# Kernel optimization log

Hardware: AMD Instinct MI355X
Metric: run time of the kernel (lower is better)

Reference implementation:

```python
import jax, jax.numpy as jnp
from jax import lax
import numpy as np

B, N, S, K, C = 8, 16384, 1024, 32, 256


def setup_inputs() -> dict:
    key = jax.random.key(0)
    ks = jax.random.split(key, 8)
    def lin(k, o, i):
        return (jax.random.normal(k, (o, i), jnp.float32) / np.sqrt(i)).astype(jnp.float32)
    return {
        "x": jax.random.normal(ks[0], (B, N, 3), jnp.float32),
        "Wqkv": lin(ks[1], 3 * C, 3), "bqkv": jnp.zeros((3 * C,), jnp.float32),
        "g1": lin(ks[2], C, C), "bg1": jnp.zeros((C,), jnp.float32),
        "g2": lin(ks[3], C, C), "bg2": jnp.zeros((C,), jnp.float32),
        "Wo": lin(ks[4], C, C), "bo": jnp.zeros((C,), jnp.float32),
        "p1": lin(ks[5], 128, 3), "bp1": jnp.zeros((128,), jnp.float32),
        "p2": lin(ks[6], C, 128), "bp2": jnp.zeros((C,), jnp.float32),
    }


def _fps(xyz, num_patches):
    # furthest point sampling, deterministic start at index 0 (matches pointnet2 CUDA op)
    b, n, _ = xyz.shape
    def body(carry, _):
        dmin, far = carry
        c = jnp.take_along_axis(xyz, far[:, None, None], axis=1)[:, 0]  # [B,3]
        d = jnp.sum((xyz - c[:, None, :]) ** 2, axis=-1)                # [B,N]
        dmin = jnp.minimum(dmin, d)
        return (dmin, jnp.argmax(dmin, axis=-1)), far
    init = (jnp.full((b, n), 1e10, xyz.dtype), jnp.zeros((b,), jnp.int32))
    _, idx = lax.scan(body, init, None, length=num_patches)
    return jnp.transpose(idx)  # [B,S]


def _gelu(x):
    return jax.nn.gelu(x, approximate=False)  # torch nn.GELU default = exact erf


def reference(x, Wqkv, bqkv, g1, bg1, g2, bg2, Wo, bo, p1, bp1, p2, bp2):
    scale = C ** (-0.5)
    fps_idx = _fps(x, S)                                        # [B,S]
    centroid = jnp.take_along_axis(x, fps_idx[..., None], axis=1)  # [B,S,3]
    # square_distance(centroid, x): [B,S,N]
    d = (jnp.sum(centroid ** 2, -1)[..., None]
         + jnp.sum(x ** 2, -1)[:, None, :]
         - 2.0 * jnp.einsum('bsc,bnc->bsn', centroid, x))
    _, knn = lax.top_k(-d, K)                                   # [B,S,K] smallest-k (== argsort[:, :, :k])
    grouped = jax.vmap(lambda pts, i: pts[i])(x, knn)           # [B,S,K,3]
    # 1x1 Conv2d over channel dim == linear on last axis
    qkv = grouped @ Wqkv.T + bqkv                               # [B,S,K,3C]
    q, k_, v = jnp.split(qkv, 3, axis=-1)
    q = q.max(axis=2); k_ = k_.max(axis=2); v = v.max(axis=2)   # [B,S,C]
    h = _gelu((q - k_) @ g1.T + bg1) @ g2.T + bg2               # fc_gamma MLP
    attn = jax.nn.softmax(h * scale, axis=-1)                   # softmax over channels
    pos = _gelu(centroid @ p1.T + bp1) @ p2.T + bp2             # [B,S,C]
    return (attn * v) @ Wo.T + bo + pos                         # [B,S,C]
```

## Files before the change

### kernel.cpp

```cpp
#include <hip/hip_runtime.h>
#include <hip/hip_bf16.h>
#include <cstdint>

#define B_ 8
#define N_ 16384
#define S_ 1024
#define K_ 32
#define C_ 256
#define RR 8

__device__ __forceinline__ float gelu_f(float x){
  return 0.5f * x * (1.0f + erff(x * 0.70710678118654752f));
}

__device__ __forceinline__ float dist2_f(float px, float py, float pz,
                                         float cx, float cy, float cz){
  float dx = px - cx, dy = py - cy, dz = pz - cz;
  return dx*dx + dy*dy + dz*dz;
}

__global__ void prep_kernel(const float* __restrict__ x,
                            const float* __restrict__ g1,
                            const float* __restrict__ g2,
                            const float* __restrict__ Wo,
                            const float* __restrict__ p2,
                            float* __restrict__ xT,
                            float* __restrict__ g1T,
                            float* __restrict__ g2T,
                            float* __restrict__ WoT,
                            float* __restrict__ p2T){
  int u = blockIdx.x * 256 + threadIdx.x;
  if (u < B_*N_){
    int b = u >> 14, n = u & (N_-1);
    const float* p = x + (size_t)u * 3;
    xT[((size_t)b*3+0)*N_ + n] = p[0];
    xT[((size_t)b*3+1)*N_ + n] = p[1];
    xT[((size_t)b*3+2)*N_ + n] = p[2];
  } else if (u < B_*N_ + 65536){
    int v = u - B_*N_; int i = v >> 8, j = v & 255;
    g1T[v] = g1[j*256 + i];
  } else if (u < B_*N_ + 2*65536){
    int v = u - B_*N_ - 65536; int i = v >> 8, j = v & 255;
    g2T[v] = g2[j*256 + i];
  } else if (u < B_*N_ + 3*65536){
    int v = u - B_*N_ - 2*65536; int i = v >> 8, j = v & 255;
    WoT[v] = Wo[j*256 + i];
  } else if (u < B_*N_ + 3*65536 + 32768){
    int v = u - B_*N_ - 3*65536; int i = v >> 8, j = v & 255;
    p2T[v] = p2[j*128 + i];
  }
}

__global__ __launch_bounds__(1024, 4) void fps_kernel(const float* __restrict__ xT,
                                                      float* __restrict__ cent){
  int b = blockIdx.x;
  int tid = threadIdx.x;
  const float* X = xT + (size_t)b*3*N_;
  const float* Y = X + N_;
  const float* Z = Y + N_;
  float px[16], py[16], pz[16], dm[16];
  #pragma unroll
  for (int i=0;i<16;i++){
    int g = i*1024 + tid;
    px[i]=X[g]; py[i]=Y[g]; pz[i]=Z[g]; dm[i]=1e10f;
  }
  __shared__ unsigned mslot[2];
  __shared__ int islot[2];
  if (tid==0){ mslot[0]=0u; mslot[1]=0u; islot[0]=0x7FFFFFFF; islot[1]=0x7FFFFFFF; }
  __syncthreads();
  int far = 0;
  for (int s=0; s<S_; s++){
    int cur = s & 1;
    float cx = X[far], cy = Y[far], cz = Z[far];
    if (tid==0){
      float* o = cent + ((size_t)b*S_ + s)*3;
      o[0]=cx; o[1]=cy; o[2]=cz;
    }
    float m = 0.0f;
    #pragma unroll
    for (int i=0;i<16;i++){
      float d = dist2_f(px[i],py[i],pz[i],cx,cy,cz);
      dm[i] = fminf(dm[i], d);
      m = fmaxf(m, dm[i]);
    }
    for (int off=32; off; off>>=1) m = fmaxf(m, __shfl_xor(m, off));
    if ((tid & 63) == 0) atomicMax(&mslot[cur], __float_as_uint(m));
    __syncthreads();
    float gm = __uint_as_float(mslot[cur]);
    if (m == gm){
      int cand = 0x7FFFFFFF;
      #pragma unroll
      for (int i=15;i>=0;i--) if (dm[i]==gm) cand = i*1024 + tid;
      if (cand != 0x7FFFFFFF) atomicMin(&islot[cur], cand);
    }
    if (tid==0){ mslot[cur^1]=0u; islot[cur^1]=0x7FFFFFFF; }
    __syncthreads();
    far = islot[cur];
  }
}

__global__ __launch_bounds__(256) void knn_qkv_kernel(const float* __restrict__ xT,
                                                      const float* __restrict__ cent,
                                                      const float* __restrict__ Wqkv,
                                                      const float* __restrict__ bqkv,
                                                      float* __restrict__ qkv){
  __shared__ unsigned hist[RR][256];
  __shared__ unsigned candB[RR][256];
  __shared__ int      candI[RR][256];
  __shared__ int      selI[RR][32];
  __shared__ float    pts[RR][32][3];
  __shared__ int      cnt[RR];
  __shared__ int      Bstar[RR];
  int tid = threadIdx.x;
  int row0 = blockIdx.x * RR;
  int b = row0 >> 10;
  const float* X = xT + (size_t)b*3*N_;
  const float* Y = X + N_;
  const float* Z = Y + N_;
  float cx[RR], cy[RR], cz[RR];
  #pragma unroll
  for (int r=0;r<RR;r++){
    const float* c = cent + ((size_t)row0 + r)*3;
    cx[r]=c[0]; cy[r]=c[1]; cz[r]=c[2];
  }
  for (int i=tid; i<RR*256; i+=256) ((unsigned*)hist)[i] = 0u;
  if (tid < RR) cnt[tid]=0;
  __syncthreads();
  for (int i=0;i<64;i++){
    int g = i*256 + tid;
    float px=X[g], py=Y[g], pz=Z[g];
    #pragma unroll
    for (int r=0;r<RR;r++){
      float d = dist2_f(px,py,pz,cx[r],cy[r],cz[r]);
      int key = (int)(__float_as_uint(d) >> 20) - 840;
      key = min(max(key,0),255);
      atomicAdd(&hist[r][key], 1u);
    }
  }
  __syncthreads();
  int w = tid >> 6, lane = tid & 63;
  for (int half=0; half<2; half++){
    int r = half*4 + w;
    uint4 h4 = ((uint4*)&hist[r][0])[lane];
    unsigned cum = h4.x + h4.y + h4.z + h4.w;
    for (int off=1; off<64; off<<=1){
      unsigned t = __shfl_up(cum, off);
      if (lane >= off) cum += t;
    }
    unsigned long long mask = __ballot(cum >= 32u);
    int lb = __ffsll((unsigned long long)mask) - 1;
    unsigned cumPrev = __shfl(cum, lb>0 ? lb-1 : 0);
    if (lane == lb){
      unsigned c0 = (lb==0) ? 0u : cumPrev;
      unsigned hh[4] = {h4.x,h4.y,h4.z,h4.w};
      int bs = lb*4 + 3;
      for (int k=0;k<4;k++){
        if (c0 + hh[k] >= 32u){ bs = lb*4 + k; break; }
        c0 += hh[k];
      }
      Bstar[r] = bs;
    }
  }
  __syncthreads();
  int bsr[RR];
  #pragma unroll
  for (int r=0;r<RR;r++) bsr[r] = min(Bstar[r]+1, 255);
  for (int i=0;i<64;i++){
    int g = i*256 + tid;
    float px=X[g], py=Y[g], pz=Z[g];
    #pragma unroll
    for (int r=0;r<RR;r++){
      float d = dist2_f(px,py,pz,cx[r],cy[r],cz[r]);
      unsigned bits = __float_as_uint(d);
      int key = min(max((int)(bits>>20) - 840, 0), 255);
      if (key <= bsr[r]){
        int pos = atomicAdd(&cnt[r], 1);
        if (pos < 256){ candB[r][pos] = bits; candI[r][pos] = g; }
      }
    }
  }
  __syncthreads();
  for (int half=0; half<2; half++){
    int r = half*4 + w;
    int L = min(cnt[r], 256);
    for (int j=lane; j<L; j+=64){
      unsigned mb = candB[r][j]; int mi = candI[r][j];
      int rank = 0;
      for (int t=0;t<L;t++){
        unsigned tb = candB[r][t]; int ti = candI[r][t];
        rank += (tb < mb || (tb == mb && ti < mi)) ? 1 : 0;
      }
      if (rank < 32) selI[r][rank] = mi;
    }
  }
  __syncthreads();
  { int r = tid >> 5, p = tid & 31;
    int g = selI[r][p];
    pts[r][p][0]=X[g]; pts[r][p][1]=Y[g]; pts[r][p][2]=Z[g]; }
  __syncthreads();
  float w0[3], w1[3], w2[3], bb[3];
  #pragma unroll
  for (int c3=0;c3<3;c3++){
    int c = tid + c3*256;
    w0[c3]=Wqkv[c*3+0]; w1[c3]=Wqkv[c*3+1]; w2[c3]=Wqkv[c*3+2]; bb[c3]=bqkv[c];
  }
  for (int r=0;r<RR;r++){
    float m0=-1e30f, m1=-1e30f, m2=-1e30f;
    #pragma unroll
    for (int p=0;p<32;p++){
      float px=pts[r][p][0], py=pts[r][p][1], pz=pts[r][p][2];
      m0 = fmaxf(m0, w0[0]*px + w1[0]*py + w2[0]*pz);
      m1 = fmaxf(m1, w0[1]*px + w1[1]*py + w2[1]*pz);
      m2 = fmaxf(m2, w0[2]*px + w1[2]*py + w2[2]*pz);
    }
    float* o = qkv + ((size_t)row0 + r)*768;
    o[tid      ] = m0 + bb[0];
    o[tid + 256] = m1 + bb[1];
    o[tid + 512] = m2 + bb[2];
  }
}

template<int KD>
__device__ __forceinline__ void gemm_tile(const float* A_, const float* __restrict__ Wt,
                                          int rb, int lane, float acc[4][4]){
  const float4* W4 = (const float4*)Wt;
  for (int i0=0; i0<(KD>>2); i0++){
    float4 wv0 = W4[(i0*4+0)*64 + lane];
    float4 wv1 = W4[(i0*4+1)*64 + lane];
    float4 wv2 = W4[(i0*4+2)*64 + lane];
    float4 wv3 = W4[(i0*4+3)*64 + lane];
    #pragma unroll
    for (int r=0;r<4;r++){
      float4 a = ((const float4*)(A_ + (size_t)(rb+r)*KD))[i0];
      acc[r][0] = fmaf(a.x,wv0.x,fmaf(a.y,wv1.x,fmaf(a.z,wv2.x,fmaf(a.w,wv3.x,acc[r][0]))));
      acc[r][1] = fmaf(a.x,wv0.y,fmaf(a.y,wv1.y,fmaf(a.z,wv2.y,fmaf(a.w,wv3.y,acc[r][1]))));
      acc[r][2] = fmaf(a.x,wv0.z,fmaf(a.y,wv1.z,fmaf(a.z,wv2.z,fmaf(a.w,wv3.z,acc[r][2]))));
      acc[r][3] = fmaf(a.x,wv0.w,fmaf(a.y,wv1.w,fmaf(a.z,wv2.w,fmaf(a.w,wv3.w,acc[r][3]))));
    }
  }
}

__global__ __launch_bounds__(512, 2) void stage2_kernel(const float* __restrict__ qkv,
                                                        const float* __restrict__ cent,
                                                        const float* __restrict__ g1T,
                                                        const float* __restrict__ bg1,
                                                        const float* __restrict__ g2T,
                                                        const float* __restrict__ bg2,
                                                        const float* __restrict__ WoT,
                                                        const float* __restrict__ bo,
                                                        const float* __restrict__ p1,
                                                        const float* __restrict__ bp1,
                                                        const float* __restrict__ p2T,
                                                        const float* __restrict__ bp2,
                                                        float* __restrict__ out){
  __shared__ float A[32][256];
  __shared__ float T[32][128];
  __shared__ float CC[32][3];
  int tid = threadIdx.x;
  int w = tid >> 6, lane = tid & 63;
  int rb = w * 4;
  int row0 = blockIdx.x * 32;
  const float4* qkv4 = (const float4*)qkv;
  #pragma unroll
  for (int t=0;t<4;t++){
    int fi = t*512 + tid;
    int r = fi >> 6, c4 = fi & 63;
    float4 q = qkv4[(size_t)(row0+r)*192 + c4];
    float4 k = qkv4[(size_t)(row0+r)*192 + 64 + c4];
    ((float4*)&A[r][0])[c4] = make_float4(q.x-k.x, q.y-k.y, q.z-k.z, q.w-k.w);
  }
  if (tid < 96) ((float*)CC)[tid] = cent[(size_t)row0*3 + tid];
  __syncthreads();
  #pragma unroll
  for (int t=0;t<8;t++){
    int e = t*512 + tid;
    int r = e >> 7, c = e & 127;
    float tv = CC[r][0]*p1[c*3+0] + CC[r][1]*p1[c*3+1] + CC[r][2]*p1[c*3+2] + bp1[c];
    T[r][c] = gelu_f(tv);
  }
  __syncthreads();
  float acc[4][4];
  #pragma unroll
  for (int r=0;r<4;r++){ acc[r][0]=0.f; acc[r][1]=0.f; acc[r][2]=0.f; acc[r][3]=0.f; }
  gemm_tile<256>(&A[0][0], g1T, rb, lane, acc);
  {
    float4 bg = ((const float4*)bg1)[lane];
    #pragma unroll
    for (int r=0;r<4;r++){
      float4 g;
      g.x = gelu_f(acc[r][0] + bg.x);
      g.y = gelu_f(acc[r][1] + bg.y);
      g.z = gelu_f(acc[r][2] + bg.z);
      g.w = gelu_f(acc[r][3] + bg.w);
      ((float4*)&A[rb+r][0])[lane] = g;
    }
  }
  #pragma unroll
  for (int r=0;r<4;r++){ acc[r][0]=0.f; acc[r][1]=0.f; acc[r][2]=0.f; acc[r][3]=0.f; }
  gemm_tile<256>(&A[0][0], g2T, rb, lane, acc);
  {
    float4 bg = ((const float4*)bg2)[lane];
    const float scale = 0.0625f;
    #pragma unroll
    for (int r=0;r<4;r++){
      float h0 = acc[r][0]+bg.x, h1 = acc[r][1]+bg.y, h2 = acc[r][2]+bg.z, h3 = acc[r][3]+bg.w;
      float mx = fmaxf(fmaxf(h0,h1), fmaxf(h2,h3));
      for (int off=1; off<64; off<<=1) mx = fmaxf(mx, __shfl_xor(mx, off));
      float e0 = __expf((h0-mx)*scale), e1 = __expf((h1-mx)*scale);
      float e2 = __expf((h2-mx)*scale), e3 = __expf((h3-mx)*scale);
      float sm = e0+e1+e2+e3;
      for (int off=1; off<64; off<<=1) sm += __shfl_xor(sm, off);
      float inv = 1.0f / sm;
      float4 v4 = qkv4[(size_t)(row0+rb+r)*192 + 128 + lane];
      ((float4*)&A[rb+r][0])[lane] =
          make_float4(e0*inv*v4.x, e1*inv*v4.y, e2*inv*v4.z, e3*inv*v4.w);
    }
  }
  #pragma unroll
  for (int r=0;r<4;r++){ acc[r][0]=0.f; acc[r][1]=0.f; acc[r][2]=0.f; acc[r][3]=0.f; }
  gemm_tile<256>(&A[0][0], WoT, rb, lane, acc);
  gemm_tile<128>(&T[0][0], p2T, rb, lane, acc);
  {
    float4 bov = ((const float4*)bo)[lane];
    float4 bpv = ((const float4*)bp2)[lane];
    #pragma unroll
    for (int r=0;r<4;r++){
      float4 o;
      o.x = acc[r][0] + bov.x + bpv.x;
      o.y = acc[r][1] + bov.y + bpv.y;
      o.z = acc[r][2] + bov.z + bpv.z;
      o.w = acc[r][3] + bov.w + bpv.w;
      ((float4*)out)[(size_t)(row0+rb+r)*64 + lane] = o;
    }
  }
}

extern "C" void kernel_launch(void* const* d_in, const int* in_sizes, int n_in,
                              void* d_out, int out_size, void* d_ws, size_t ws_size,
                              hipStream_t stream) {
  const float* x    = (const float*)d_in[0];
  const float* Wqkv = (const float*)d_in[1];
  const float* bqkv = (const float*)d_in[2];
  const float* g1   = (const float*)d_in[3];
  const float* bg1  = (const float*)d_in[4];
  const float* g2   = (const float*)d_in[5];
  const float* bg2  = (const float*)d_in[6];
  const float* Wo   = (const float*)d_in[7];
  const float* bo   = (const float*)d_in[8];
  const float* p1   = (const float*)d_in[9];
  const float* bp1  = (const float*)d_in[10];
  const float* p2   = (const float*)d_in[11];
  const float* bp2  = (const float*)d_in[12];
  float* out = (float*)d_out;
  float* ws = (float*)d_ws;

  float* xT   = ws;
  float* cent = xT + 393216;
  float* qkv  = cent + 24576;
  float* g1T  = qkv + 6291456;
  float* g2T  = g1T + 65536;
  float* WoT  = g2T + 65536;
  float* p2T  = WoT + 65536;

  hipLaunchKernelGGL(prep_kernel, dim3(1408), dim3(256), 0, stream,
                     x, g1, g2, Wo, p2, xT, g1T, g2T, WoT, p2T);
  hipLaunchKernelGGL(fps_kernel, dim3(B_), dim3(1024), 0, stream, xT, cent);
  hipLaunchKernelGGL(knn_qkv_kernel, dim3(B_*S_/RR), dim3(256), 0, stream,
                     xT, cent, Wqkv, bqkv, qkv);
  hipLaunchKernelGGL(stage2_kernel, dim3(B_*S_/32), dim3(512), 0, stream,
                     qkv, cent, g1T, bg1, g2T, bg2, WoT, bo, p1, bp1, p2T, bp2, out);
}
```

Measured before the change: 1.900 ms.

## Restructure FPS kernel with 512 threads, per-wave max slots, and packed float4 points

The FPS kernel now runs 512 threads per batch, each holding 32 points, and reads points from a new packed float4 array written by the prep kernel. The global max is found by writing per-wave maxima to shared memory and reducing them, which replaces the shared atomicMax slot. The next centroid comes from one float4 load instead of three strided loads. Centroids are buffered in shared memory and written out at the end. The intent is to cut per-iteration synchronisation and atomic costs in this serial 1024-step loop, at the price of more registers per thread and an extra workspace buffer.

```diff
diff --git a/kernel.cpp b/kernel.cpp
--- a/kernel.cpp
+++ b/kernel.cpp
@@ -28,14 +28,17 @@
                             float* __restrict__ g1T,
                             float* __restrict__ g2T,
                             float* __restrict__ WoT,
-                            float* __restrict__ p2T){
+                            float* __restrict__ p2T,
+                            float4* __restrict__ xP){
   int u = blockIdx.x * 256 + threadIdx.x;
   if (u < B_*N_){
     int b = u >> 14, n = u & (N_-1);
     const float* p = x + (size_t)u * 3;
-    xT[((size_t)b*3+0)*N_ + n] = p[0];
-    xT[((size_t)b*3+1)*N_ + n] = p[1];
-    xT[((size_t)b*3+2)*N_ + n] = p[2];
+    float X = p[0], Y = p[1], Z = p[2];
+    xT[((size_t)b*3+0)*N_ + n] = X;
+    xT[((size_t)b*3+1)*N_ + n] = Y;
+    xT[((size_t)b*3+2)*N_ + n] = Z;
+    xP[u] = make_float4(X, Y, Z, X*X + Y*Y + Z*Z);
   } else if (u < B_*N_ + 65536){
     int v = u - B_*N_; int i = v >> 8, j = v & 255;
     g1T[v] = g1[j*256 + i];
@@ -51,52 +54,67 @@
   }
 }
 
-__global__ __launch_bounds__(1024, 4) void fps_kernel(const float* __restrict__ xT,
-                                                      float* __restrict__ cent){
+__global__ __launch_bounds__(512, 2) void fps_kernel(const float4* __restrict__ xP,
+                                                     float* __restrict__ cent){
   int b = blockIdx.x;
   int tid = threadIdx.x;
-  const float* X = xT + (size_t)b*3*N_;
-  const float* Y = X + N_;
-  const float* Z = Y + N_;
-  float px[16], py[16], pz[16], dm[16];
-  #pragma unroll
-  for (int i=0;i<16;i++){
-    int g = i*1024 + tid;
-    px[i]=X[g]; py[i]=Y[g]; pz[i]=Z[g]; dm[i]=1e10f;
-  }
-  __shared__ unsigned mslot[2];
+  int w = tid >> 6, lane = tid & 63;
+  const float4* P = xP + (size_t)b * N_;
+  float px[32], py[32], pz[32], dm[32];
+  #pragma unroll
+  for (int i=0;i<32;i++){
+    float4 p = P[i*512 + tid];
+    px[i]=p.x; py[i]=p.y; pz[i]=p.z; dm[i]=1e10f;
+  }
+  __shared__ float wmax[8];
   __shared__ int islot[2];
-  if (tid==0){ mslot[0]=0u; mslot[1]=0u; islot[0]=0x7FFFFFFF; islot[1]=0x7FFFFFFF; }
-  __syncthreads();
-  int far = 0;
+  __shared__ float centb[S_*3];
+  if (tid < 2) islot[tid] = 0x7FFFFFFF;
+  __syncthreads();
+  float4 c4 = P[0];
   for (int s=0; s<S_; s++){
     int cur = s & 1;
-    float cx = X[far], cy = Y[far], cz = Z[far];
-    if (tid==0){
-      float* o = cent + ((size_t)b*S_ + s)*3;
-      o[0]=cx; o[1]=cy; o[2]=cz;
-    }
-    float m = 0.0f;
-    #pragma unroll
-    for (int i=0;i<16;i++){
-      float d = dist2_f(px[i],py[i],pz[i],cx,cy,cz);
+    if (tid == 0){
+      centb[s*3+0]=c4.x; centb[s*3+1]=c4.y; centb[s*3+2]=c4.z;
+    }
+    float cx=c4.x, cy=c4.y, cz=c4.z;
+    #pragma unroll
+    for (int i=0;i<32;i++){
+      float dx=px[i]-cx, dy=py[i]-cy, dz=pz[i]-cz;
+      float d = fmaf(dz,dz, fmaf(dy,dy, dx*dx));
       dm[i] = fminf(dm[i], d);
-      m = fmaxf(m, dm[i]);
-    }
-    for (int off=32; off; off>>=1) m = fmaxf(m, __shfl_xor(m, off));
-    if ((tid & 63) == 0) atomicMax(&mslot[cur], __float_as_uint(m));
+    }
+    float tt[16];
+    #pragma unroll
+    for (int i=0;i<16;i++) tt[i] = fmaxf(dm[2*i], dm[2*i+1]);
+    #pragma unroll
+    for (int i=0;i<8;i++) tt[i] = fmaxf(tt[i], tt[i+8]);
+    #pragma unroll
+    for (int i=0;i<4;i++) tt[i] = fmaxf(tt[i], tt[i+4]);
+    float ml = fmaxf(fmaxf(tt[0],tt[1]), fmaxf(tt[2],tt[3]));
+    float wm = ml;
+    for (int off=32; off; off>>=1) wm = fmaxf(wm, __shfl_xor(wm, off));
+    if (lane == 0) wmax[w] = wm;
+    if (tid == 0) islot[cur^1] = 0x7FFFFFFF;
     __syncthreads();
-    float gm = __uint_as_float(mslot[cur]);
-    if (m == gm){
-      int cand = 0x7FFFFFFF;
+    float g0 = fmaxf(fmaxf(wmax[0],wmax[1]), fmaxf(wmax[2],wmax[3]));
+    float g1 = fmaxf(fmaxf(wmax[4],wmax[5]), fmaxf(wmax[6],wmax[7]));
+    float gm = fmaxf(g0, g1);
+    if (wm == gm){
+      int cidx = 0x7FFFFFFF;
       #pragma unroll
-      for (int i=15;i>=0;i--) if (dm[i]==gm) cand = i*1024 + tid;
-      if (cand != 0x7FFFFFFF) atomicMin(&islot[cur], cand);
-    }
-    if (tid==0){ mslot[cur^1]=0u; islot[cur^1]=0x7FFFFFFF; }
+      for (int i=0;i<32;i++){
+        int idxi = i*512 + tid;
+        cidx = min(cidx, (dm[i]==gm) ? idxi : 0x7FFFFFFF);
+      }
+      if (cidx != 0x7FFFFFFF) atomicMin(&islot[cur], cidx);
+    }
     __syncthreads();
-    far = islot[cur];
-  }
+    int far = islot[cur];
+    c4 = P[far];
+  }
+  __syncthreads();
+  for (int i = tid; i < S_*3; i += 512) cent[(size_t)b*S_*3 + i] = centb[i];
 }
 
 __global__ __launch_bounds__(256) void knn_qkv_kernel(const float* __restrict__ xT,
@@ -361,10 +379,11 @@
   float* g2T  = g1T + 65536;
   float* WoT  = g2T + 65536;
   float* p2T  = WoT + 65536;
+  float4* xP  = (float4*)(p2T + 32768);
 
   hipLaunchKernelGGL(prep_kernel, dim3(1408), dim3(256), 0, stream,
-                     x, g1, g2, Wo, p2, xT, g1T, g2T, WoT, p2T);
-  hipLaunchKernelGGL(fps_kernel, dim3(B_), dim3(1024), 0, stream, xT, cent);
+                     x, g1, g2, Wo, p2, xT, g1T, g2T, WoT, p2T, xP);
+  hipLaunchKernelGGL(fps_kernel, dim3(B_), dim3(512), 0, stream, xP, cent);
   hipLaunchKernelGGL(knn_qkv_kernel, dim3(B_*S_/RR), dim3(256), 0, stream,
                      xT, cent, Wqkv, bqkv, qkv);
   hipLaunchKernelGGL(stage2_kernel, dim3(B_*S_/32), dim3(512), 0, stream,
```

Result: faster. 1.668 ms (-12.2%).
